# Kernel optimization log

Hardware: AMD Instinct MI355X
Metric: run time of the kernel (lower is better)

The kernel has to match this reference:

```python
import jax, jax.numpy as jnp
import numpy as np

N_NODES = 100000
N_EDGES = 1600000
IN_CH = 500
H1, C1 = 8, 8           # layer 1: 8 heads x 8 dims, concat -> 64
H2, C2 = 8, 3           # layer 2: 8 heads x 3 classes, mean over heads
NEG_SLOPE = 0.2         # PyG GATConv default


def gat_layer(x, src, dst, W, a_src, a_dst, b, concat):
    """PyG-style GATConv (self-loops already included in src/dst)."""
    N = x.shape[0]
    H, C = a_src.shape
    xw = (x @ W).reshape(N, H, C)                      # [N,H,C]
    al_src = jnp.einsum('nhc,hc->nh', xw, a_src)       # [N,H]
    al_dst = jnp.einsum('nhc,hc->nh', xw, a_dst)       # [N,H]
    e = jax.nn.leaky_relu(al_src[src] + al_dst[dst], NEG_SLOPE)  # [E,H]
    # segment softmax over incoming edges of each destination node
    m = jax.lax.stop_gradient(jax.ops.segment_max(e, dst, num_segments=N))
    ex = jnp.exp(e - m[dst])
    s = jax.ops.segment_sum(ex, dst, num_segments=N)
    alpha = ex / (s[dst] + 1e-16)                      # [E,H]
    out = jax.ops.segment_sum(alpha[:, :, None] * xw[src], dst, num_segments=N)  # [N,H,C]
    out = out.reshape(N, H * C) if concat else out.mean(axis=1)
    return out + b


def setup_inputs() -> dict:
    key = jax.random.key(0)
    ks = jax.random.split(key, 10)
    x = jax.random.normal(ks[0], (N_NODES, IN_CH), dtype=jnp.float32)
    edge_index = jax.random.randint(ks[1], (2, N_EDGES), 0, N_NODES, dtype=jnp.int64)
    sc1 = 1.0 / np.sqrt(IN_CH)
    sc2 = 1.0 / np.sqrt(H1 * C1)
    W1 = jax.random.normal(ks[2], (IN_CH, H1 * C1), dtype=jnp.float32) * sc1
    a1_src = jax.random.normal(ks[3], (H1, C1), dtype=jnp.float32) * 0.1
    a1_dst = jax.random.normal(ks[4], (H1, C1), dtype=jnp.float32) * 0.1
    b1 = jnp.zeros((H1 * C1,), dtype=jnp.float32)
    W2 = jax.random.normal(ks[5], (H1 * C1, H2 * C2), dtype=jnp.float32) * sc2
    a2_src = jax.random.normal(ks[6], (H2, C2), dtype=jnp.float32) * 0.1
    a2_dst = jax.random.normal(ks[7], (H2, C2), dtype=jnp.float32) * 0.1
    b2 = jnp.zeros((C2,), dtype=jnp.float32)
    return {"x": x, "W1": W1, "a1_src": a1_src, "a1_dst": a1_dst, "b1": b1,
            "W2": W2, "a2_src": a2_src, "a2_dst": a2_dst, "b2": b2,
            "edge_index": edge_index}


def reference(x, W1, a1_src, a1_dst, b1, W2, a2_src, a2_dst, b2, edge_index):
    N = x.shape[0]
    loop = jnp.arange(N, dtype=edge_index.dtype)   # PyG add_self_loops=True
    src = jnp.concatenate([edge_index[0], loop])
    dst = jnp.concatenate([edge_index[1], loop])
    h = jax.nn.elu(gat_layer(x, src, dst, W1, a1_src, a1_dst, b1, concat=True))
    out = gat_layer(h, src, dst, W2, a2_src, a2_dst, b2, concat=False)
    return jax.nn.softmax(out, axis=1)
```

## Files before the change

kernel.cpp:

```cpp
#include <hip/hip_runtime.h>
#include <math.h>

#define N_NODESC 100000
#define N_EDGESC 1600000
#define E_TOT    1700000
#define IN_CH    500
#define KPAD     512
#define D1 64
#define D2 24
#define D2P 32
#define NBKT 391
#define CAP  5120
#define EPB  4096
#define NPB  416
#define WPB  32

typedef __attribute__((ext_vector_type(8))) short short8;
typedef __attribute__((ext_vector_type(4))) float f32x4;

__device__ inline short f2bf(float f) {
    unsigned u = __float_as_uint(f);
    u += 0x7fffu + ((u >> 16) & 1u);
    return (short)(u >> 16);
}
__device__ inline unsigned pkbf(float a, float b) {
    const unsigned ua = __float_as_uint(a) + 0x8000u;
    const unsigned ub = __float_as_uint(b) + 0x8000u;
    return __builtin_amdgcn_perm(ub, ua, 0x07060302u);
}
__device__ inline float bflo(unsigned u) { return __uint_as_float(u << 16); }
__device__ inline float bfhi(unsigned u) { return __uint_as_float(u & 0xffff0000u); }

__global__ __launch_bounds__(256) void k_part2(const int* __restrict__ ei,
                                               int* __restrict__ gcnt,
                                               int* __restrict__ tmp,
                                               const float* __restrict__ W1,
                                               short* __restrict__ wT) {
    const int t = threadIdx.x;
    if (blockIdx.x >= NPB) {
        const int wb = blockIdx.x - NPB;
#pragma unroll
        for (int r = 0; r < 4; r++) {
            const int idx = wb * 1024 + r * 256 + t;
            const int n = idx >> 9, k = idx & (KPAD - 1);
            wT[idx] = (k < IN_CH) ? f2bf(W1[k * D1 + n]) : (short)0;
        }
        return;
    }
    __shared__ int hist[NBKT];
    __shared__ int lbase[NBKT];
    const int e0 = blockIdx.x * EPB;
    for (int i = t; i < NBKT; i += 256) hist[i] = 0;
    __syncthreads();
    int se[16], de[16], mo[16];
#pragma unroll
    for (int i = 0; i < 16; i++) {
        const int e = e0 + i * 256 + t;
        int s = -1, d = 0;
        if (e < E_TOT) {
            if (e < N_EDGESC) { s = ei[e]; d = ei[N_EDGESC + e]; }
            else { s = d = e - N_EDGESC; }
        }
        se[i] = s; de[i] = d;
        mo[i] = (s >= 0) ? atomicAdd(&hist[d >> 8], 1) : 0;
    }
    __syncthreads();
    for (int i = t; i < NBKT; i += 256)
        lbase[i] = hist[i] ? (i * CAP + atomicAdd(&gcnt[i * 32], hist[i])) : 0;
    __syncthreads();
#pragma unroll
    for (int i = 0; i < 16; i++) {
        if (se[i] >= 0) {
            const int b = de[i] >> 8;
            const int idx = lbase[b] + mo[i];
            if (idx < (b + 1) * CAP)
                tmp[idx] = se[i] | ((de[i] & 255) << 17);
        }
    }
}

__global__ __launch_bounds__(256) void k_bucket2(const int* __restrict__ gcnt,
                                                 const int* __restrict__ tmp,
                                                 int* __restrict__ off,
                                                 int* __restrict__ srt) {
    __shared__ int se[CAP];
    __shared__ int cnts[256];
    __shared__ int sc[256];
    __shared__ int lcur[256];
    __shared__ int red[4];
    __shared__ int sbase;
    const int b = blockIdx.x;
    const int t = threadIdx.x;
    const int cnt = min(gcnt[b * 32], CAP);

    int pre = 0;
    if (t < b) pre += min(gcnt[t * 32], CAP);
    if (t + 256 < b) pre += min(gcnt[(t + 256) * 32], CAP);
#pragma unroll
    for (int m = 1; m < 64; m <<= 1) pre += __shfl_xor(pre, m, 64);
    if ((t & 63) == 0) red[t >> 6] = pre;
    cnts[t] = 0;
    __syncthreads();
    if (t == 0) sbase = red[0] + red[1] + red[2] + red[3];
    __syncthreads();
    const int base = sbase;

    for (int i = t; i < cnt; i += 256) {
        const int p = tmp[b * CAP + i];
        se[i] = p;
        atomicAdd(&cnts[p >> 17], 1);
    }
    __syncthreads();
    sc[t] = cnts[t];
    __syncthreads();
    for (int d = 1; d < 256; d <<= 1) {
        const int u = (t >= d) ? sc[t - d] : 0;
        __syncthreads();
        sc[t] += u;
        __syncthreads();
    }
    const int excl = base + sc[t] - cnts[t];
    const int nodeBase = b << 8;
    const int nNodes = min(256, N_NODESC - nodeBase);
    if (t < nNodes) off[nodeBase + t] = excl;
    lcur[t] = excl;
    if (b == 0 && t == 0) off[N_NODESC] = E_TOT;
    __syncthreads();
    for (int i = t; i < cnt; i += 256) {
        const int p = se[i];
        const int pos = atomicAdd(&lcur[p >> 17], 1);
        srt[pos] = p & 0x1FFFF;
    }
}

__global__ __launch_bounds__(256) void k_gemm1(const float* __restrict__ x,
                                               const short* __restrict__ wT,
                                               const float* __restrict__ a1s,
                                               const float* __restrict__ a1d,
                                               short* __restrict__ xw1b,
                                               float* __restrict__ al1s,
                                               float* __restrict__ al1d) {
    __shared__ short xs[32 * 520];
    const int t = threadIdx.x;
    const int rowBase = blockIdx.x * 32;
    const int r = t >> 3, j = t & 7;
    const float* xr = x + (long)(rowBase + r) * IN_CH;
    short* xrow = xs + r * 520;
#pragma unroll
    for (int i = 0; i < 16; i++) {
        const int c = j + i * 8;
        if (c < 125) {
            const float4 v = *(const float4*)(xr + c * 4);
            const unsigned lo = pkbf(v.x, v.y);
            const unsigned hi = pkbf(v.z, v.w);
            *(uint2*)(xrow + c * 4) = make_uint2(lo, hi);
        }
    }
    if (j < 6) *(unsigned*)(xrow + 500 + j * 2) = 0u;
    __syncthreads();

    const int lane = t & 63, wv = t >> 6;
    const int m = lane & 15, kg = lane >> 4;
    f32x4 acc[2];
    acc[0] = (f32x4){0.f, 0.f, 0.f, 0.f};
    acc[1] = (f32x4){0.f, 0.f, 0.f, 0.f};
    const short* wcol = wT + (wv * 16 + m) * KPAD;
#pragma unroll
    for (int k0 = 0; k0 < KPAD; k0 += 32) {
        const short8 bf = *(const short8*)(wcol + k0 + kg * 8);
#pragma unroll
        for (int mf = 0; mf < 2; mf++) {
            const short8 af = *(const short8*)(xs + (mf * 16 + m) * 520 + k0 + kg * 8);
            acc[mf] = __builtin_amdgcn_mfma_f32_16x16x32_bf16(af, bf, acc[mf], 0, 0, 0);
        }
    }
    const int col = wv * 16 + m;
    const float as = a1s[col];
    const float ad = a1d[col];
    const int hh = wv * 2 + (m >> 3);
#pragma unroll
    for (int mf = 0; mf < 2; mf++) {
#pragma unroll
        for (int jj = 0; jj < 4; jj++) {
            const int row = rowBase + mf * 16 + kg * 4 + jj;
            const float v = acc[mf][jj];
            xw1b[(long)row * D1 + col] = f2bf(v);
            float ts = v * as, td = v * ad;
            ts += __shfl_xor(ts, 1, 64); td += __shfl_xor(td, 1, 64);
            ts += __shfl_xor(ts, 2, 64); td += __shfl_xor(td, 2, 64);
            ts += __shfl_xor(ts, 4, 64); td += __shfl_xor(td, 4, 64);
            if ((m & 7) == 0) {
                al1s[row * 8 + hh] = ts;
                al1d[row * 8 + hh] = td;
            }
        }
    }
}

__global__ __launch_bounds__(256) void k_gat1(const int* __restrict__ off,
                                              const int* __restrict__ srt_src,
                                              const float* __restrict__ al1s,
                                              const float* __restrict__ al1d,
                                              const short* __restrict__ xw1b,
                                              const float* __restrict__ b1,
                                              const float* __restrict__ W2,
                                              const float* __restrict__ a2s,
                                              const float* __restrict__ a2d,
                                              float* __restrict__ xw2,
                                              float* __restrict__ al2s,
                                              float* __restrict__ al2d) {
    __shared__ float w2s[D1 * D2];
    __shared__ float hrow[4][D1];
    const int tid = threadIdx.x;
    for (int i = tid; i < D1 * D2; i += 256) w2s[i] = W2[i];
    __syncthreads();

    const int lane = tid & 63;
    const int wid = tid >> 6;
    const int n = blockIdx.x * 4 + wid;
    const int e8 = lane >> 3;
    const int hd = lane & 7;

    const float ald = al1d[n * 8 + hd];
    const int kend = off[n + 1];

    float4 a0 = make_float4(0.f, 0.f, 0.f, 0.f);
    float4 a1 = make_float4(0.f, 0.f, 0.f, 0.f);
    float ssum = 0.f;
    int k = off[n] + e8;
    int s = (k < kend) ? srt_src[k] : -1;
    while (s >= 0) {
        const int kn = k + 8;
        const int sn = (kn < kend) ? srt_src[kn] : -1;
        float ev = al1s[s * 8 + hd] + ald;
        ev = ev > 0.f ? ev : 0.2f * ev;
        const float ex = __expf(ev);
        const uint4 v = *(const uint4*)(xw1b + (long)s * D1 + hd * 8);
        a0.x += ex * bflo(v.x); a0.y += ex * bfhi(v.x);
        a0.z += ex * bflo(v.y); a0.w += ex * bfhi(v.y);
        a1.x += ex * bflo(v.z); a1.y += ex * bfhi(v.z);
        a1.z += ex * bflo(v.w); a1.w += ex * bfhi(v.w);
        ssum += ex;
        k = kn; s = sn;
    }
#pragma unroll
    for (int mm = 8; mm < 64; mm <<= 1) {
        a0.x += __shfl_xor(a0.x, mm, 64); a0.y += __shfl_xor(a0.y, mm, 64);
        a0.z += __shfl_xor(a0.z, mm, 64); a0.w += __shfl_xor(a0.w, mm, 64);
        a1.x += __shfl_xor(a1.x, mm, 64); a1.y += __shfl_xor(a1.y, mm, 64);
        a1.z += __shfl_xor(a1.z, mm, 64); a1.w += __shfl_xor(a1.w, mm, 64);
        ssum  += __shfl_xor(ssum,  mm, 64);
    }
    const float inv = 1.0f / (ssum + 1e-16f);
    const float4 bb0 = *(const float4*)(b1 + hd * 8);
    const float4 bb1 = *(const float4*)(b1 + hd * 8 + 4);
    float4 r0, r1;
    r0.x = a0.x * inv + bb0.x; r0.x = r0.x > 0.f ? r0.x : expm1f(r0.x);
    r0.y = a0.y * inv + bb0.y; r0.y = r0.y > 0.f ? r0.y : expm1f(r0.y);
    r0.z = a0.z * inv + bb0.z; r0.z = r0.z > 0.f ? r0.z : expm1f(r0.z);
    r0.w = a0.w * inv + bb0.w; r0.w = r0.w > 0.f ? r0.w : expm1f(r0.w);
    r1.x = a1.x * inv + bb1.x; r1.x = r1.x > 0.f ? r1.x : expm1f(r1.x);
    r1.y = a1.y * inv + bb1.y; r1.y = r1.y > 0.f ? r1.y : expm1f(r1.y);
    r1.z = a1.z * inv + bb1.z; r1.z = r1.z > 0.f ? r1.z : expm1f(r1.z);
    r1.w = a1.w * inv + bb1.w; r1.w = r1.w > 0.f ? r1.w : expm1f(r1.w);
    if (e8 == 0) {
        *(float4*)(&hrow[wid][hd * 8])     = r0;
        *(float4*)(&hrow[wid][hd * 8 + 4]) = r1;
    }
    const int half = lane / 24;
    const int j2 = lane - half * 24;
    const int cb = (half == 1) ? 32 : 0;
    float o = 0.f;
#pragma unroll
    for (int c4 = 0; c4 < 8; c4++) {
        const float4 hv = *(const float4*)(&hrow[wid][cb + c4 * 4]);
        const float* wr = w2s + (cb + c4 * 4) * D2 + j2;
        o += hv.x * wr[0] + hv.y * wr[D2] + hv.z * wr[2 * D2] + hv.w * wr[3 * D2];
    }
    const int src2 = (lane < 24) ? lane + 24 : lane;
    o += __shfl(o, src2, 64);
    if (lane < 24) {
        const int h3 = j2 / 3;
        xw2[(long)n * D2P + h3 * 4 + (j2 - 3 * h3)] = o;
    }
    const float ps = o * a2s[j2];
    const float pd = o * a2d[j2];
    const int hb = 3 * (lane & 7);
    const float s3 = __shfl(ps, hb, 64) + __shfl(ps, hb + 1, 64) + __shfl(ps, hb + 2, 64);
    const float d3 = __shfl(pd, hb, 64) + __shfl(pd, hb + 1, 64) + __shfl(pd, hb + 2, 64);
    if (lane < 8) {
        al2s[n * 8 + lane] = s3;
        al2d[n * 8 + lane] = d3;
    }
}

__global__ __launch_bounds__(256) void k_gat2(const int* __restrict__ off,
                                              const int* __restrict__ srt_src,
                                              const float* __restrict__ al2s,
                                              const float* __restrict__ al2d,
                                              const float* __restrict__ xw2,
                                              const float* __restrict__ b2,
                                              float* __restrict__ out) {
    const int tid = threadIdx.x;
    const int lane = tid & 63;
    const int wid = tid >> 6;
    const int n = blockIdx.x * 4 + wid;
    const int e8 = lane >> 3;
    const int hd = lane & 7;

    const float ald = al2d[n * 8 + hd];
    const int kend = off[n + 1];

    float ax = 0.f, ay = 0.f, az = 0.f, ssum = 0.f;
    int k = off[n] + e8;
    int s = (k < kend) ? srt_src[k] : -1;
    while (s >= 0) {
        const int kn = k + 8;
        const int sn = (kn < kend) ? srt_src[kn] : -1;
        float ev = al2s[s * 8 + hd] + ald;
        ev = ev > 0.f ? ev : 0.2f * ev;
        const float ex = __expf(ev);
        const float4 v = *(const float4*)(xw2 + (long)s * D2P + hd * 4);
        ax += ex * v.x; ay += ex * v.y; az += ex * v.z;
        ssum += ex;
        k = kn; s = sn;
    }
#pragma unroll
    for (int mm = 8; mm < 64; mm <<= 1) {
        ax += __shfl_xor(ax, mm, 64);
        ay += __shfl_xor(ay, mm, 64);
        az += __shfl_xor(az, mm, 64);
        ssum += __shfl_xor(ssum, mm, 64);
    }
    const float inv = 1.0f / (ssum + 1e-16f);
    float mx = ax * inv, my = ay * inv, mz = az * inv;
#pragma unroll
    for (int mm = 1; mm < 8; mm <<= 1) {
        mx += __shfl_xor(mx, mm, 64);
        my += __shfl_xor(my, mm, 64);
        mz += __shfl_xor(mz, mm, 64);
    }
    const float l0 = mx * 0.125f + b2[0];
    const float l1 = my * 0.125f + b2[1];
    const float l2 = mz * 0.125f + b2[2];
    const float mmax = fmaxf(l0, fmaxf(l1, l2));
    const float ee0 = expf(l0 - mmax), ee1 = expf(l1 - mmax), ee2 = expf(l2 - mmax);
    const float dinv = 1.0f / (ee0 + ee1 + ee2);
    if (lane < 3) {
        const float p = (lane == 0) ? ee0 : (lane == 1) ? ee1 : ee2;
        out[(long)n * 3 + lane] = p * dinv;
    }
}

extern "C" void kernel_launch(void* const* d_in, const int* in_sizes, int n_in,
                              void* d_out, int out_size, void* d_ws, size_t ws_size,
                              hipStream_t stream) {
    const float* x   = (const float*)d_in[0];
    const float* W1  = (const float*)d_in[1];
    const float* a1s = (const float*)d_in[2];
    const float* a1d = (const float*)d_in[3];
    const float* b1  = (const float*)d_in[4];
    const float* W2  = (const float*)d_in[5];
    const float* a2s = (const float*)d_in[6];
    const float* a2d = (const float*)d_in[7];
    const float* b2  = (const float*)d_in[8];
    const int*   ei  = (const int*)d_in[9];
    float* out = (float*)d_out;

    float* ws   = (float*)d_ws;
    float* xw2  = ws;
    float* al1s = xw2  + 3200000;
    float* al1d = al1s + 800000;
    float* al2s = al1d + 800000;
    float* al2d = al2s + 800000;
    short* xw1b = (short*)(al2d + 800000);
    int* off    = (int*)(xw1b + 6400000);
    int* gcnt   = off + 100004;
    int* srt    = gcnt + NBKT * 32;
    short* wT   = (short*)(srt + 1700000);
    int* tmp    = (int*)xw2;

    hipMemsetAsync(gcnt, 0, (size_t)NBKT * 32 * sizeof(int), stream);

    k_part2<<<NPB + WPB, 256, 0, stream>>>(ei, gcnt, tmp, W1, wT);
    k_bucket2<<<NBKT, 256, 0, stream>>>(gcnt, tmp, off, srt);
    k_gemm1<<<N_NODESC / 32, 256, 0, stream>>>(x, wT, a1s, a1d, xw1b, al1s, al1d);
    k_gat1<<<N_NODESC / 4, 256, 0, stream>>>(off, srt, al1s, al1d, xw1b, b1,
                                             W2, a2s, a2d, xw2, al2s, al2d);
    k_gat2<<<N_NODESC / 4, 256, 0, stream>>>(off, srt, al2s, al2d, xw2, b2, out);
}
```

Baseline: 483.4 us.

## Fuse edge partition with GEMM1, software-prefetch gathers, pack al2s into xw2 padding

Replaces the memset plus weight-transpose branch with a small init kernel. The edge partition and the layer-1 GEMM now run as one launch, so partition blocks and GEMM blocks execute concurrently. The bucket sort uses 512 threads per block. Both GAT aggregation loops prefetch the next neighbour's features, and layer-2 source attention logits are stored in the unused 4th slot of each padded xw2 head, so one float4 gather replaces two loads. The aim is fewer launches, overlap between independent stages, and hidden gather latency, at the cost of more registers and a tmp/xw2 aliasing dependence that relies on launch ordering.

```diff
diff --git a/kernel.cpp b/kernel.cpp
--- a/kernel.cpp
+++ b/kernel.cpp
@@ -13,7 +13,7 @@
 #define CAP  5120
 #define EPB  4096
 #define NPB  416
-#define WPB  32
+#define GEMB 3125
 
 typedef __attribute__((ext_vector_type(8))) short short8;
 typedef __attribute__((ext_vector_type(4))) float f32x4;
@@ -31,118 +31,65 @@
 __device__ inline float bflo(unsigned u) { return __uint_as_float(u << 16); }
 __device__ inline float bfhi(unsigned u) { return __uint_as_float(u & 0xffff0000u); }
 
-__global__ __launch_bounds__(256) void k_part2(const int* __restrict__ ei,
-                                               int* __restrict__ gcnt,
-                                               int* __restrict__ tmp,
-                                               const float* __restrict__ W1,
-                                               short* __restrict__ wT) {
-    const int t = threadIdx.x;
-    if (blockIdx.x >= NPB) {
-        const int wb = blockIdx.x - NPB;
-#pragma unroll
-        for (int r = 0; r < 4; r++) {
-            const int idx = wb * 1024 + r * 256 + t;
-            const int n = idx >> 9, k = idx & (KPAD - 1);
-            wT[idx] = (k < IN_CH) ? f2bf(W1[k * D1 + n]) : (short)0;
-        }
-        return;
-    }
-    __shared__ int hist[NBKT];
-    __shared__ int lbase[NBKT];
-    const int e0 = blockIdx.x * EPB;
-    for (int i = t; i < NBKT; i += 256) hist[i] = 0;
-    __syncthreads();
-    int se[16], de[16], mo[16];
-#pragma unroll
-    for (int i = 0; i < 16; i++) {
-        const int e = e0 + i * 256 + t;
-        int s = -1, d = 0;
-        if (e < E_TOT) {
-            if (e < N_EDGESC) { s = ei[e]; d = ei[N_EDGESC + e]; }
-            else { s = d = e - N_EDGESC; }
-        }
-        se[i] = s; de[i] = d;
-        mo[i] = (s >= 0) ? atomicAdd(&hist[d >> 8], 1) : 0;
-    }
-    __syncthreads();
-    for (int i = t; i < NBKT; i += 256)
-        lbase[i] = hist[i] ? (i * CAP + atomicAdd(&gcnt[i * 32], hist[i])) : 0;
-    __syncthreads();
-#pragma unroll
-    for (int i = 0; i < 16; i++) {
-        if (se[i] >= 0) {
-            const int b = de[i] >> 8;
-            const int idx = lbase[b] + mo[i];
-            if (idx < (b + 1) * CAP)
-                tmp[idx] = se[i] | ((de[i] & 255) << 17);
-        }
-    }
-}
-
-__global__ __launch_bounds__(256) void k_bucket2(const int* __restrict__ gcnt,
-                                                 const int* __restrict__ tmp,
-                                                 int* __restrict__ off,
-                                                 int* __restrict__ srt) {
-    __shared__ int se[CAP];
-    __shared__ int cnts[256];
-    __shared__ int sc[256];
-    __shared__ int lcur[256];
-    __shared__ int red[4];
-    __shared__ int sbase;
-    const int b = blockIdx.x;
-    const int t = threadIdx.x;
-    const int cnt = min(gcnt[b * 32], CAP);
-
-    int pre = 0;
-    if (t < b) pre += min(gcnt[t * 32], CAP);
-    if (t + 256 < b) pre += min(gcnt[(t + 256) * 32], CAP);
-#pragma unroll
-    for (int m = 1; m < 64; m <<= 1) pre += __shfl_xor(pre, m, 64);
-    if ((t & 63) == 0) red[t >> 6] = pre;
-    cnts[t] = 0;
-    __syncthreads();
-    if (t == 0) sbase = red[0] + red[1] + red[2] + red[3];
-    __syncthreads();
-    const int base = sbase;
-
-    for (int i = t; i < cnt; i += 256) {
-        const int p = tmp[b * CAP + i];
-        se[i] = p;
-        atomicAdd(&cnts[p >> 17], 1);
-    }
-    __syncthreads();
-    sc[t] = cnts[t];
-    __syncthreads();
-    for (int d = 1; d < 256; d <<= 1) {
-        const int u = (t >= d) ? sc[t - d] : 0;
-        __syncthreads();
-        sc[t] += u;
-        __syncthreads();
-    }
-    const int excl = base + sc[t] - cnts[t];
-    const int nodeBase = b << 8;
-    const int nNodes = min(256, N_NODESC - nodeBase);
-    if (t < nNodes) off[nodeBase + t] = excl;
-    lcur[t] = excl;
-    if (b == 0 && t == 0) off[N_NODESC] = E_TOT;
-    __syncthreads();
-    for (int i = t; i < cnt; i += 256) {
-        const int p = se[i];
-        const int pos = atomicAdd(&lcur[p >> 17], 1);
-        srt[pos] = p & 0x1FFFF;
-    }
-}
-
-__global__ __launch_bounds__(256) void k_gemm1(const float* __restrict__ x,
-                                               const short* __restrict__ wT,
-                                               const float* __restrict__ a1s,
-                                               const float* __restrict__ a1d,
-                                               short* __restrict__ xw1b,
-                                               float* __restrict__ al1s,
-                                               float* __restrict__ al1d) {
+__global__ __launch_bounds__(256) void k_init(int* __restrict__ gcnt,
+                                              const float* __restrict__ W1,
+                                              short* __restrict__ wT) {
+    const int tid = blockIdx.x * 256 + threadIdx.x;
+    for (int i = tid; i < D1 * KPAD; i += 16384) {
+        const int n = i >> 9, k = i & (KPAD - 1);
+        wT[i] = (k < IN_CH) ? f2bf(W1[k * D1 + n]) : (short)0;
+    }
+    for (int i = tid; i < NBKT * 32; i += 16384) gcnt[i] = 0;
+}
+
+__global__ __launch_bounds__(256) void k_pg(const int* __restrict__ ei,
+                                            int* __restrict__ gcnt,
+                                            int* __restrict__ tmp,
+                                            const float* __restrict__ x,
+                                            const short* __restrict__ wT,
+                                            const float* __restrict__ a1s,
+                                            const float* __restrict__ a1d,
+                                            short* __restrict__ xw1b,
+                                            float* __restrict__ al1s,
+                                            float* __restrict__ al1d) {
     __shared__ short xs[32 * 520];
     const int t = threadIdx.x;
-    const int rowBase = blockIdx.x * 32;
+
+    if (blockIdx.x < NPB) {
+        int* hist  = (int*)xs;
+        int* lbase = hist + NBKT;
+        const int e0 = blockIdx.x * EPB;
+        for (int i = t; i < NBKT; i += 256) hist[i] = 0;
+        __syncthreads();
+        int se[16], de[16], mo[16];
+#pragma unroll
+        for (int i = 0; i < 16; i++) {
+            const int e = e0 + i * 256 + t;
+            int s = -1, d = 0;
+            if (e < E_TOT) {
+                if (e < N_EDGESC) { s = ei[e]; d = ei[N_EDGESC + e]; }
+                else { s = d = e - N_EDGESC; }
+            }
+            se[i] = s; de[i] = d;
+            mo[i] = (s >= 0) ? atomicAdd(&hist[d >> 8], 1) : 0;
+        }
+        __syncthreads();
+        for (int i = t; i < NBKT; i += 256)
+            lbase[i] = hist[i] ? (i * CAP + atomicAdd(&gcnt[i * 32], hist[i])) : 0;
+        __syncthreads();
+#pragma unroll
+        for (int i = 0; i < 16; i++) {
+            if (se[i] >= 0) {
+                const int b = de[i] >> 8;
+                const int idx = lbase[b] + mo[i];
+                if (idx < (b + 1) * CAP)
+                    tmp[idx] = se[i] | ((de[i] & 255) << 17);
+            }
+        }
+        return;
+    }
+
+    const int rowBase = (blockIdx.x - NPB) * 32;
     const int r = t >> 3, j = t & 7;
     const float* xr = x + (long)(rowBase + r) * IN_CH;
     short* xrow = xs + r * 520;
@@ -197,6 +144,65 @@
     }
 }
 
+__global__ __launch_bounds__(512) void k_bucket2(const int* __restrict__ gcnt,
+                                                 const int* __restrict__ tmp,
+                                                 int* __restrict__ off,
+                                                 int* __restrict__ srt) {
+    __shared__ int se[CAP];
+    __shared__ int cnts[256];
+    __shared__ int sc[256];
+    __shared__ int lcur[256];
+    __shared__ int red[8];
+    __shared__ int sbase;
+    const int b = blockIdx.x;
+    const int t = threadIdx.x;
+    const int cnt = min(gcnt[b * 32], CAP);
+
+    int pre = (t < b) ? min(gcnt[t * 32], CAP) : 0;
+#pragma unroll
+    for (int m = 1; m < 64; m <<= 1) pre += __shfl_xor(pre, m, 64);
+    if ((t & 63) == 0) red[t >> 6] = pre;
+    if (t < 256) cnts[t] = 0;
+    __syncthreads();
+    if (t == 0) {
+        int sb = 0;
+#pragma unroll
+        for (int i = 0; i < 8; i++) sb += red[i];
+        sbase = sb;
+    }
+    __syncthreads();
+    const int base = sbase;
+
+    for (int i = t; i < cnt; i += 512) {
+        const int p = tmp[b * CAP + i];
+        se[i] = p;
+        atomicAdd(&cnts[p >> 17], 1);
+    }
+    __syncthreads();
+    if (t < 256) sc[t] = cnts[t];
+    __syncthreads();
+    for (int d = 1; d < 256; d <<= 1) {
+        const int u = (t >= d && t < 256) ? sc[t - d] : 0;
+        __syncthreads();
+        if (t < 256) sc[t] += u;
+        __syncthreads();
+    }
+    const int nodeBase = b << 8;
+    const int nNodes = min(256, N_NODESC - nodeBase);
+    if (t < 256) {
+        const int excl = base + sc[t] - cnts[t];
+        if (t < nNodes) off[nodeBase + t] = excl;
+        lcur[t] = excl;
+    }
+    if (b == 0 && t == 0) off[N_NODESC] = E_TOT;
+    __syncthreads();
+    for (int i = t; i < cnt; i += 512) {
+        const int p = se[i];
+        const int pos = atomicAdd(&lcur[p >> 17], 1);
+        srt[pos] = p & 0x1FFFF;
+    }
+}
+
 __global__ __launch_bounds__(256) void k_gat1(const int* __restrict__ off,
                                               const int* __restrict__ srt_src,
                                               const float* __restrict__ al1s,
@@ -207,7 +213,6 @@
                                               const float* __restrict__ a2s,
                                               const float* __restrict__ a2d,
                                               float* __restrict__ xw2,
-                                              float* __restrict__ al2s,
                                               float* __restrict__ al2d) {
     __shared__ float w2s[D1 * D2];
     __shared__ float hrow[4][D1];
@@ -229,19 +234,30 @@
     float ssum = 0.f;
     int k = off[n] + e8;
     int s = (k < kend) ? srt_src[k] : -1;
+    float al = 0.f;
+    uint4 v = make_uint4(0u, 0u, 0u, 0u);
+    if (s >= 0) {
+        al = al1s[s * 8 + hd];
+        v = *(const uint4*)(xw1b + (long)s * D1 + hd * 8);
+    }
     while (s >= 0) {
         const int kn = k + 8;
         const int sn = (kn < kend) ? srt_src[kn] : -1;
-        float ev = al1s[s * 8 + hd] + ald;
+        float aln = 0.f;
+        uint4 vn = v;
+        if (sn >= 0) {
+            aln = al1s[sn * 8 + hd];
+            vn = *(const uint4*)(xw1b + (long)sn * D1 + hd * 8);
+        }
+        float ev = al + ald;
         ev = ev > 0.f ? ev : 0.2f * ev;
         const float ex = __expf(ev);
-        const uint4 v = *(const uint4*)(xw1b + (long)s * D1 + hd * 8);
         a0.x += ex * bflo(v.x); a0.y += ex * bfhi(v.x);
         a0.z += ex * bflo(v.y); a0.w += ex * bfhi(v.y);
         a1.x += ex * bflo(v.z); a1.y += ex * bfhi(v.z);
         a1.z += ex * bflo(v.w); a1.w += ex * bfhi(v.w);
         ssum += ex;
-        k = kn; s = sn;
+        k = kn; s = sn; al = aln; v = vn;
     }
 #pragma unroll
     for (int mm = 8; mm < 64; mm <<= 1) {
@@ -289,14 +305,13 @@
     const float s3 = __shfl(ps, hb, 64) + __shfl(ps, hb + 1, 64) + __shfl(ps, hb + 2, 64);
     const float d3 = __shfl(pd, hb, 64) + __shfl(pd, hb + 1, 64) + __shfl(pd, hb + 2, 64);
     if (lane < 8) {
-        al2s[n * 8 + lane] = s3;
+        xw2[(long)n * D2P + lane * 4 + 3] = s3;
         al2d[n * 8 + lane] = d3;
     }
 }
 
 __global__ __launch_bounds__(256) void k_gat2(const int* __restrict__ off,
                                               const int* __restrict__ srt_src,
-                                              const float* __restrict__ al2s,
                                               const float* __restrict__ al2d,
                                               const float* __restrict__ xw2,
                                               const float* __restrict__ b2,
@@ -314,16 +329,19 @@
     float ax = 0.f, ay = 0.f, az = 0.f, ssum = 0.f;
     int k = off[n] + e8;
     int s = (k < kend) ? srt_src[k] : -1;
+    float4 v = make_float4(0.f, 0.f, 0.f, 0.f);
+    if (s >= 0) v = *(const float4*)(xw2 + (long)s * D2P + hd * 4);
     while (s >= 0) {
         const int kn = k + 8;
         const int sn = (kn < kend) ? srt_src[kn] : -1;
-        float ev = al2s[s * 8 + hd] + ald;
+        float4 vn = v;
+        if (sn >= 0) vn = *(const float4*)(xw2 + (long)sn * D2P + hd * 4);
+        float ev = v.w + ald;
         ev = ev > 0.f ? ev : 0.2f * ev;
         const float ex = __expf(ev);
-        const float4 v = *(const float4*)(xw2 + (long)s * D2P + hd * 4);
         ax += ex * v.x; ay += ex * v.y; az += ex * v.z;
         ssum += ex;
-        k = kn; s = sn;
+        k = kn; s = sn; v = vn;
     }
 #pragma unroll
     for (int mm = 8; mm < 64; mm <<= 1) {
@@ -371,8 +389,7 @@
     float* xw2  = ws;
     float* al1s = xw2  + 3200000;
     float* al1d = al1s + 800000;
-    float* al2s = al1d + 800000;
-    float* al2d = al2s + 800000;
+    float* al2d = al1d + 800000;
     short* xw1b = (short*)(al2d + 800000);
     int* off    = (int*)(xw1b + 6400000);
     int* gcnt   = off + 100004;
@@ -380,12 +397,11 @@
     short* wT   = (short*)(srt + 1700000);
     int* tmp    = (int*)xw2;
 
-    hipMemsetAsync(gcnt, 0, (size_t)NBKT * 32 * sizeof(int), stream);
-
-    k_part2<<<NPB + WPB, 256, 0, stream>>>(ei, gcnt, tmp, W1, wT);
-    k_bucket2<<<NBKT, 256, 0, stream>>>(gcnt, tmp, off, srt);
-    k_gemm1<<<N_NODESC / 32, 256, 0, stream>>>(x, wT, a1s, a1d, xw1b, al1s, al1d);
+    k_init<<<64, 256, 0, stream>>>(gcnt, W1, wT);
+    k_pg<<<NPB + GEMB, 256, 0, stream>>>(ei, gcnt, tmp, x, wT, a1s, a1d,
+                                         xw1b, al1s, al1d);
+    k_bucket2<<<NBKT, 512, 0, stream>>>(gcnt, tmp, off, srt);
     k_gat1<<<N_NODESC / 4, 256, 0, stream>>>(off, srt, al1s, al1d, xw1b, b1,
-                                             W2, a2s, a2d, xw2, al2s, al2d);
-    k_gat2<<<N_NODESC / 4, 256, 0, stream>>>(off, srt, al2s, al2d, xw2, b2, out);
-}
+                                             W2, a2s, a2d, xw2, al2d);
+    k_gat2<<<N_NODESC / 4, 256, 0, stream>>>(off, srt, al2d, xw2, b2, out);
+}
```

Measured after the change: 467.0 us. 3.4% less time.
